# Optimization experiments

Hardware: AMD Instinct MI355X
Metric: run time of the kernel (lower is better)

## Reference

```python
import jax, jax.numpy as jnp
import numpy as np
import math

B, S, D, H = 2, 2048, 1024, 16

def setup_inputs() -> dict:
    key = jax.random.key(0)
    ks = jax.random.split(key, 13)
    def lin(kw, kb, out_d, in_d):
        W = jax.random.normal(kw, (out_d, in_d), dtype=jnp.float32) * 0.02
        b = jax.random.normal(kb, (out_d,), dtype=jnp.float32) * 0.02
        return W, b
    Wq, bq = lin(ks[0], ks[1], D, D)
    Wk, bk = lin(ks[2], ks[3], D, D)
    Wv, bv = lin(ks[4], ks[5], D, D)
    Wo, bo = lin(ks[6], ks[7], D, D)
    query = jax.random.normal(ks[8], (B, S, D), dtype=jnp.float32)
    key_t = jax.random.normal(ks[9], (B, S, D), dtype=jnp.float32)
    value = jax.random.normal(ks[10], (B, S, D), dtype=jnp.float32)
    src_mask = jax.random.randint(ks[11], (B, S), 0, 2).astype(bool)  # True = masked out
    return {"query": query, "key": key_t, "value": value, "src_mask": src_mask,
            "Wq": Wq, "bq": bq, "Wk": Wk, "bk": bk, "Wv": Wv, "bv": bv,
            "Wo": Wo, "bo": bo, "nhead": H}

def reference(query, key, value, src_mask, Wq, bq, Wk, bk, Wv, bv, Wo, bo, nhead):
    b, s, d = query.shape
    hd = d // nhead
    scale = 1.0 / math.sqrt(hd)
    def split_heads(x):  # [b,s,d] -> [b,h,s,hd]
        return x.reshape(b, -1, nhead, hd).transpose(0, 2, 1, 3)
    q = split_heads(query @ Wq.T + bq)
    k = split_heads(key @ Wk.T + bk)
    v = split_heads(value @ Wv.T + bv)
    scores = jnp.einsum('bhqe,bhke->bhqk', q, k) * scale  # [b,h,s,s]
    # mask True -> -9e9, broadcast over heads and query positions (matches repeat)
    scores = jnp.where(src_mask[:, None, None, :], jnp.float32(-9e9), scores)
    probs = jax.nn.softmax(scores, axis=-1)
    # dropout is identity in eval mode
    out = jnp.einsum('bhqk,bhke->bhqe', probs, v)  # [b,h,s,hd]
    out = out.transpose(0, 2, 1, 3).reshape(b, s, d)
    out = out @ Wo.T + bo
    return out
```

## Files before the change

### kernel.cpp

```cpp
#include <hip/hip_runtime.h>
#include <hip/hip_bf16.h>
#include <cstdint>
#include <cstddef>

#define B_ 2
#define S_ 2048
#define D_ 1024
#define H_ 16
#define HD_ 64
#define M_ 4096

typedef __attribute__((ext_vector_type(8))) short short8;
typedef __attribute__((ext_vector_type(4))) float floatx4;
typedef __attribute__((ext_vector_type(16))) float f32x16;
typedef __attribute__((ext_vector_type(2))) int intx2;

__device__ __forceinline__ floatx4 mfma32(short8 a, short8 b, floatx4 c) {
    return __builtin_amdgcn_mfma_f32_16x16x32_bf16(a, b, c, 0, 0, 0);
}
__device__ __forceinline__ f32x16 mfma3216(short8 a, short8 b, f32x16 c) {
    return __builtin_amdgcn_mfma_f32_32x32x16_bf16(a, b, c, 0, 0, 0);
}

__device__ __forceinline__ void gload_lds16(const __hip_bfloat16* g, __hip_bfloat16* lds_base) {
    __builtin_amdgcn_global_load_lds(
        (const __attribute__((address_space(1))) void*)g,
        (__attribute__((address_space(3))) void*)lds_base, 16, 0, 0);
}

__device__ __forceinline__ int pkbf(float a, float b) {
    union { __hip_bfloat162 h; int i; } u;
    u.h = __float22bfloat162_rn({a, b});
    return u.i;
}
__device__ __forceinline__ void pl32swap(int& a, int& b) {
    intx2 r = __builtin_amdgcn_permlane32_swap(a, b, false, false);
    a = r.x; b = r.y;
}

__global__ __launch_bounds__(256) void cvt_all_kernel(
    const float* __restrict__ q, const float* __restrict__ k, const float* __restrict__ v,
    const float* __restrict__ wq, const float* __restrict__ wk,
    const float* __restrict__ wv, const float* __restrict__ wo,
    const int* __restrict__ mask,
    __hip_bfloat16* __restrict__ dstIn,
    __hip_bfloat16* __restrict__ dstW,
    float* __restrict__ fbias)
{
    const int bid = blockIdx.x;
    const int tid = threadIdx.x;
    const size_t SZ_IN = (size_t)M_ * D_;
    const size_t SZ_W  = (size_t)D_ * D_;
    if (bid < 12288) {
        int z = bid >> 12, xb = bid & 4095;
        const float* src = z == 0 ? q : z == 1 ? k : v;
        __hip_bfloat16* d = dstIn + (size_t)z * SZ_IN;
        int i = (xb * 256 + tid) * 4;
        float4 val = *(const float4*)(src + i);
        union { __hip_bfloat16 h[4]; uint2 u; } cv;
        cv.h[0] = __float2bfloat16(val.x); cv.h[1] = __float2bfloat16(val.y);
        cv.h[2] = __float2bfloat16(val.z); cv.h[3] = __float2bfloat16(val.w);
        *(uint2*)(d + i) = cv.u;
    } else if (bid < 16384) {
        int r  = bid - 12288;
        int z  = r >> 10, xb = r & 1023;
        const float* src = z == 0 ? wq : z == 1 ? wk : z == 2 ? wv : wo;
        __hip_bfloat16* d = dstW + (size_t)z * SZ_W;
        int i = (xb * 256 + tid) * 4;
        float4 val = *(const float4*)(src + i);
        union { __hip_bfloat16 h[4]; uint2 u; } cv;
        cv.h[0] = __float2bfloat16(val.x); cv.h[1] = __float2bfloat16(val.y);
        cv.h[2] = __float2bfloat16(val.z); cv.h[3] = __float2bfloat16(val.w);
        *(uint2*)(d + i) = cv.u;
    } else {
        int i = ((bid - 16384) * 256 + tid) * 4;
        int4 m = *(const int4*)(mask + i);
        float4 o;
        o.x = m.x ? -100000.0f : 0.0f;
        o.y = m.y ? -100000.0f : 0.0f;
        o.z = m.z ? -100000.0f : 0.0f;
        o.w = m.w ? -100000.0f : 0.0f;
        *(float4*)(fbias + i) = o;
    }
}

template <int MODE>
__device__ __forceinline__ void gemm_core(
    const __hip_bfloat16* __restrict__ A,
    const __hip_bfloat16* __restrict__ W,
    const float* __restrict__ bias,
    void* __restrict__ Cout,
    __hip_bfloat16* __restrict__ smem,
    int m0, int n0, int N)
{
    __hip_bfloat16* As = smem;
    __hip_bfloat16* Bs = smem + 128 * 32;
    const int K = D_;
    const int tid  = threadIdx.x;
    const int wave = tid >> 6;
    const int lane = tid & 63;
    const int quad = lane >> 4;
    const int l15  = lane & 15;
    const int wm   = (wave & 1) * 64;
    const int wn   = (wave >> 1) * 64;
    const int srow = lane >> 2;
    const int scol = (lane & 3) * 8;

    floatx4 acc[4][4];
#pragma unroll
    for (int i = 0; i < 4; i++)
#pragma unroll
        for (int j = 0; j < 4; j++) {
            floatx4 z = {0.f, 0.f, 0.f, 0.f};
            acc[i][j] = z;
        }

    for (int k0 = 0; k0 < K; k0 += 32) {
        __syncthreads();
#pragma unroll
        for (int t = 0; t < 2; t++) {
            int r0 = wave * 32 + t * 16;
            gload_lds16(A + (size_t)(m0 + r0 + srow) * K + k0 + scol, As + r0 * 32);
            gload_lds16(W + (size_t)(n0 + r0 + srow) * K + k0 + scol, Bs + r0 * 32);
        }
        __syncthreads();

        short8 afr[4], bfr[4];
#pragma unroll
        for (int i = 0; i < 4; i++)
            afr[i] = *(const short8*)(As + (wm + i * 16 + l15) * 32 + quad * 8);
#pragma unroll
        for (int j = 0; j < 4; j++)
            bfr[j] = *(const short8*)(Bs + (wn + j * 16 + l15) * 32 + quad * 8);
#pragma unroll
        for (int i = 0; i < 4; i++)
#pragma unroll
            for (int j = 0; j < 4; j++)
                acc[i][j] = mfma32(afr[i], bfr[j], acc[i][j]);
    }

    if constexpr (MODE == 1) {
#pragma unroll
        for (int j = 0; j < 4; j++) {
            int col = n0 + wn + j * 16 + l15;
            int h = col >> 6, e = col & 63;
            float bv = bias[col];
#pragma unroll
            for (int i = 0; i < 4; i++) {
                int s0 = m0 + wm + i * 16 + quad * 4;
                int bb = s0 >> 11, sl = s0 & 2047;
                union { __hip_bfloat16 hx[4]; uint2 u; } pk;
#pragma unroll
                for (int r = 0; r < 4; r++)
                    pk.hx[r] = __float2bfloat16(acc[i][j][r] + bv);
                *(uint2*)((__hip_bfloat16*)Cout + (((size_t)bb * H_ + h) * HD_ + e) * S_ + sl) = pk.u;
            }
        }
    } else {
#pragma unroll
        for (int j = 0; j < 4; j++) {
            int col = n0 + wn + j * 16 + l15;
            float bv = bias[col];
#pragma unroll
            for (int i = 0; i < 4; i++) {
#pragma unroll
                for (int r = 0; r < 4; r++) {
                    int rowg = m0 + wm + i * 16 + quad * 4 + r;
                    ((__hip_bfloat16*)Cout)[(size_t)rowg * N + col] =
                        __float2bfloat16(acc[i][j][r] + bv);
                }
            }
        }
    }
}

__global__ __launch_bounds__(256) void qkv_gemm_kernel(
    const __hip_bfloat16* __restrict__ qb, const __hip_bfloat16* __restrict__ kb,
    const __hip_bfloat16* __restrict__ vb,
    const __hip_bfloat16* __restrict__ Wqb, const __hip_bfloat16* __restrict__ Wkb,
    const __hip_bfloat16* __restrict__ Wvb,
    const float* __restrict__ bq, const float* __restrict__ bk, const float* __restrict__ bv,
    __hip_bfloat16* __restrict__ Qp, __hip_bfloat16* __restrict__ Kp,
    __hip_bfloat16* __restrict__ Vt)
{
    __shared__ __hip_bfloat16 smem[2 * 128 * 32] __attribute__((aligned(16)));
    const int z = blockIdx.z;
    const __hip_bfloat16* A = z == 0 ? qb : z == 1 ? kb : vb;
    const __hip_bfloat16* W = z == 0 ? Wqb : z == 1 ? Wkb : Wvb;
    const float* bias = z == 0 ? bq : z == 1 ? bk : bv;
    int lin  = blockIdx.y * 8 + blockIdx.x;
    int work = (lin & 7) * 32 + (lin >> 3);
    int m0 = (work >> 3) * 128, n0 = (work & 7) * 128;
    if (z < 2) gemm_core<0>(A, W, bias, z == 0 ? (void*)Qp : (void*)Kp, smem, m0, n0, D_);
    else       gemm_core<1>(A, W, bias, (void*)Vt, smem, m0, n0, D_);
}

__global__ __launch_bounds__(256) void oproj_gemm_kernel(
    const __hip_bfloat16* __restrict__ A, const __hip_bfloat16* __restrict__ W,
    const float* __restrict__ bias, float* __restrict__ out)
{
    __shared__ __hip_bfloat16 As[64 * 32]  __attribute__((aligned(16)));
    __shared__ __hip_bfloat16 Bs[128 * 32] __attribute__((aligned(16)));
    const int K = D_, N = D_;
    const int tid  = threadIdx.x;
    int lin  = blockIdx.y * 8 + blockIdx.x;
    int work = (lin & 7) * 64 + (lin >> 3);
    const int m0   = (work >> 3) * 64;
    const int n0   = (work & 7) * 128;
    const int wave = tid >> 6;
    const int lane = tid & 63;
    const int quad = lane >> 4;
    const int l15  = lane & 15;
    const int wm   = (wave & 1) * 32;
    const int wn   = (wave >> 1) * 64;
    const int srow = lane >> 2;
    const int scol = (lane & 3) * 8;

    floatx4 acc[2][4];
#pragma unroll
    for (int i = 0; i < 2; i++)
#pragma unroll
        for (int j = 0; j < 4; j++) {
            floatx4 z = {0.f, 0.f, 0.f, 0.f};
            acc[i][j] = z;
        }

    for (int k0 = 0; k0 < K; k0 += 32) {
        __syncthreads();
        {
            int ra = wave * 16;
            gload_lds16(A + (size_t)(m0 + ra + srow) * K + k0 + scol, As + ra * 32);
#pragma unroll
            for (int t = 0; t < 2; t++) {
                int rb = wave * 32 + t * 16;
                gload_lds16(W + (size_t)(n0 + rb + srow) * K + k0 + scol, Bs + rb * 32);
            }
        }
        __syncthreads();

        short8 afr[2], bfr[4];
#pragma unroll
        for (int i = 0; i < 2; i++)
            afr[i] = *(const short8*)(As + (wm + i * 16 + l15) * 32 + quad * 8);
#pragma unroll
        for (int j = 0; j < 4; j++)
            bfr[j] = *(const short8*)(Bs + (wn + j * 16 + l15) * 32 + quad * 8);
#pragma unroll
        for (int i = 0; i < 2; i++)
#pragma unroll
            for (int j = 0; j < 4; j++)
                acc[i][j] = mfma32(afr[i], bfr[j], acc[i][j]);
    }

#pragma unroll
    for (int j = 0; j < 4; j++) {
        int col = n0 + wn + j * 16 + l15;
        float bv = bias[col];
#pragma unroll
        for (int i = 0; i < 2; i++) {
#pragma unroll
            for (int r = 0; r < 4; r++) {
                int rowg = m0 + wm + i * 16 + quad * 4 + r;
                out[(size_t)rowg * N + col] = acc[i][j][r] + bv;
            }
        }
    }
}

#define LDP 72
#define NTK (S_ / 64)
#define KVBUF (64 * LDP)
__global__ __launch_bounds__(512, 4) void flash_attn_kernel(
    const __hip_bfloat16* __restrict__ Q,
    const __hip_bfloat16* __restrict__ Kp,
    const __hip_bfloat16* __restrict__ Vt,
    const float* __restrict__ fbias,
    __hip_bfloat16* __restrict__ O)
{
    __shared__ __hip_bfloat16 smem[4 * KVBUF] __attribute__((aligned(16)));

    const int tid  = threadIdx.x;
    int lin  = blockIdx.y * 16 + blockIdx.x;
    int work = (lin & 7) * 64 + (lin >> 3);
    const int q0   = (work & 15) * 128;
    const int bh   = work >> 4;
    const int b    = bh >> 4;
    const int h    = bh & 15;
    const int warp = tid >> 6;
    const int qw   = warp & 3;
    const int kvh  = warp >> 2;
    const int lane = tid & 63;
    const int l31  = lane & 31;
    const int hi   = lane >> 5;
    const float kSc = 0.18033688f;

    const size_t baseQ = ((size_t)b * S_ + q0) * D_ + (size_t)h * HD_;
#pragma unroll
    for (int c = tid; c < 1024; c += 512) {
        int row = c >> 3, kc = c & 7;
        *(uint4*)(smem + row * LDP + kc * 8) =
            *(const uint4*)(Q + baseQ + (size_t)row * D_ + kc * 8);
    }
    __syncthreads();
    short8 qb[4];
#pragma unroll
    for (int ks = 0; ks < 4; ks++)
        qb[ks] = *(const short8*)(smem + (qw * 32 + l31) * LDP + ks * 16 + hi * 8);
    __syncthreads();

    const float* brow = fbias + b * S_;
    const __hip_bfloat16* VtBase = Vt + (size_t)bh * HD_ * S_;
    const size_t baseKrow = (size_t)b * S_ * D_ + (size_t)h * HD_;

    const int r0  = tid >> 3;
    const int kc0 = (tid & 7) * 8;

    uint4 kreg, vreg;
    auto issue = [&](int kv0) {
        kreg = *(const uint4*)(Kp + baseKrow + (size_t)(kv0 + r0) * D_ + kc0);
        vreg = *(const uint4*)(VtBase + (size_t)r0 * S_ + kv0 + kc0);
    };
    auto commit = [&](int pb) {
        *(uint4*)(smem + pb * KVBUF + r0 * LDP + kc0) = kreg;
        *(uint4*)(smem + (2 + pb) * KVBUF + r0 * LDP + kc0) = vreg;
    };

    issue(0);
    commit(0);
    __syncthreads();

    float lsum = 0.f;
    f32x16 o_acc[2];
#pragma unroll
    for (int hdb = 0; hdb < 2; hdb++)
#pragma unroll
        for (int r = 0; r < 16; r++) o_acc[hdb][r] = 0.f;

    short8 pa_p[2];
    short8 vfr_p[4];

    for (int t = 0; t < NTK; ++t) {
        if (t) __syncthreads();

        if (t + 1 < NTK) issue((t + 1) * 64);

        const __hip_bfloat16* Ks  = smem + (t & 1) * KVBUF;
        const __hip_bfloat16* Vts = smem + (2 + (t & 1)) * KVBUF;

        f32x16 z;
#pragma unroll
        for (int r = 0; r < 16; r++) z[r] = 0.f;
        __builtin_amdgcn_s_setprio(1);
#pragma unroll
        for (int ks = 0; ks < 4; ks++) {
            short8 ka = *(const short8*)(Ks + (kvh * 32 + l31) * LDP + ks * 16 + hi * 8);
            z = mfma3216(ka, qb[ks], z);
        }
        if (t) {
#pragma unroll
            for (int hdb = 0; hdb < 2; hdb++)
#pragma unroll
                for (int ksl = 0; ksl < 2; ksl++)
                    o_acc[hdb] = mfma3216(pa_p[ksl], vfr_p[hdb * 2 + ksl], o_acc[hdb]);
        }
        __builtin_amdgcn_s_setprio(0);

#pragma unroll
        for (int ksl = 0; ksl < 2; ksl++) {
            const float* bb = brow + t * 64 + kvh * 32 + ksl * 16 + hi * 4;
            floatx4 b0 = *(const floatx4*)(bb);
            floatx4 b1 = *(const floatx4*)(bb + 8);
            float p[8];
#pragma unroll
            for (int i = 0; i < 8; i++) {
                float bias = (i < 4) ? b0[i & 3] : b1[i & 3];
                p[i] = __builtin_amdgcn_exp2f(z[ksl * 8 + i] * kSc + bias);
            }
            lsum += ((p[0] + p[1]) + (p[2] + p[3])) + ((p[4] + p[5]) + (p[6] + p[7]));
            int w0 = pkbf(p[0], p[1]);
            int w2 = pkbf(p[4], p[5]);
            int w1 = pkbf(p[2], p[3]);
            int w3 = pkbf(p[6], p[7]);
            pl32swap(w0, w2);
            pl32swap(w1, w3);
            union { int w[4]; short8 s; } fr;
            fr.w[0] = w0; fr.w[1] = w1; fr.w[2] = w2; fr.w[3] = w3;
            pa_p[ksl] = fr.s;
        }

#pragma unroll
        for (int hdb = 0; hdb < 2; hdb++)
#pragma unroll
            for (int ksl = 0; ksl < 2; ksl++)
                vfr_p[hdb * 2 + ksl] = *(const short8*)(Vts + (hdb * 32 + l31) * LDP +
                                                        kvh * 32 + ksl * 16 + hi * 8);

        if (t + 1 < NTK) commit((t + 1) & 1);
    }

    __builtin_amdgcn_s_setprio(1);
#pragma unroll
    for (int hdb = 0; hdb < 2; hdb++)
#pragma unroll
        for (int ksl = 0; ksl < 2; ksl++)
            o_acc[hdb] = mfma3216(pa_p[ksl], vfr_p[hdb * 2 + ksl], o_acc[hdb]);
    __builtin_amdgcn_s_setprio(0);

    __syncthreads();
    float* ored = (float*)smem;
    float* lred = (float*)smem + 8192;
    if (kvh == 1) {
#pragma unroll
        for (int hdb = 0; hdb < 2; hdb++)
#pragma unroll
            for (int r = 0; r < 16; r++)
                ored[(hdb * 16 + r) * 256 + qw * 64 + lane] = o_acc[hdb][r];
        lred[qw * 64 + lane] = lsum;
    }
    __syncthreads();
    if (kvh == 0) {
#pragma unroll
        for (int hdb = 0; hdb < 2; hdb++)
#pragma unroll
            for (int r = 0; r < 16; r++)
                o_acc[hdb][r] += ored[(hdb * 16 + r) * 256 + qw * 64 + lane];
        float ls = lsum + lred[qw * 64 + lane];
        ls += __shfl_xor(ls, 32);
        float inv = 1.0f / ls;

        const size_t baseO = ((size_t)b * S_ + q0 + qw * 32) * D_ + (size_t)h * HD_;
#pragma unroll
        for (int r = 0; r < 16; r++) {
            int crow = (r & 3) + 8 * (r >> 2) + 4 * hi;
            float iv = __shfl(inv, crow);
#pragma unroll
            for (int hdb = 0; hdb < 2; hdb++)
                O[baseO + (size_t)crow * D_ + hdb * 32 + l31] =
                    __float2bfloat16(o_acc[hdb][r] * iv);
        }
    }
}

extern "C" void kernel_launch(void* const* d_in, const int* in_sizes, int n_in,
                              void* d_out, int out_size, void* d_ws, size_t ws_size,
                              hipStream_t stream) {
    const float* query = (const float*)d_in[0];
    const float* key   = (const float*)d_in[1];
    const float* value = (const float*)d_in[2];
    const int*   mask  = (const int*)d_in[3];
    const float* Wq    = (const float*)d_in[4];
    const float* bq    = (const float*)d_in[5];
    const float* Wk    = (const float*)d_in[6];
    const float* bk    = (const float*)d_in[7];
    const float* Wv    = (const float*)d_in[8];
    const float* bv    = (const float*)d_in[9];
    const float* Wo    = (const float*)d_in[10];
    const float* bo    = (const float*)d_in[11];
    float* out = (float*)d_out;

    const size_t SZ_IN = (size_t)M_ * D_;
    const size_t SZ_W  = (size_t)D_ * D_;
    __hip_bfloat16* qb  = (__hip_bfloat16*)d_ws;
    __hip_bfloat16* kb  = qb  + SZ_IN;
    __hip_bfloat16* vb  = kb  + SZ_IN;
    __hip_bfloat16* Wqb = vb  + SZ_IN;
    __hip_bfloat16* Wkb = Wqb + SZ_W;
    __hip_bfloat16* Wvb = Wkb + SZ_W;
    __hip_bfloat16* Wob = Wvb + SZ_W;
    __hip_bfloat16* Qp  = Wob + SZ_W;
    __hip_bfloat16* Kp  = Qp  + SZ_IN;
    __hip_bfloat16* Vt  = Kp  + SZ_IN;
    float*          fb  = (float*)(Vt + SZ_IN);

    cvt_all_kernel<<<dim3(16388), 256, 0, stream>>>(
        query, key, value, Wq, Wk, Wv, Wo, mask, qb, Wqb, fb);

    qkv_gemm_kernel<<<dim3(D_ / 128, M_ / 128, 3), 256, 0, stream>>>(
        qb, kb, vb, Wqb, Wkb, Wvb, bq, bk, bv, Qp, Kp, Vt);

    flash_attn_kernel<<<dim3(S_ / 128, B_ * H_), 512, 0, stream>>>(Qp, Kp, Vt, fb, Qp);

    oproj_gemm_kernel<<<dim3(D_ / 128, M_ / 64), 256, 0, stream>>>(Qp, Wob, bo, out);
}
```

Before: 221.7 us.

## Double the flash-attention KV tile to 128 and drop cross-iteration PV software pipelining

The flash attention loop now processes 128 keys per iteration instead of 64, halving the number of barriers and global-to-LDS staging rounds. Each iteration runs two QK^T MFMA chains and interleaves softmax packing with the PV MFMAs, reading V fragments straight from LDS rather than carrying P and V fragments over to the next iteration. This raises register and LDS use (two prefetch registers each for K and V, larger buffers) and gives up the previous overlap of last iteration's PV with the current QK^T.

New measurement: 271.3 us. +22.4%, slower.

```diff
diff --git a/kernel.cpp b/kernel.cpp
--- a/kernel.cpp
+++ b/kernel.cpp
@@ -267,9 +267,37 @@
     }
 }
 
-#define LDP 72
-#define NTK (S_ / 64)
-#define KVBUF (64 * LDP)
+__device__ __forceinline__ void sm_pack(const f32x16& z, const float* brow_sub, int hi,
+                                        float kSc, float& lsum, short8* pa) {
+#pragma unroll
+    for (int ksl = 0; ksl < 2; ksl++) {
+        const float* bb = brow_sub + ksl * 16 + hi * 4;
+        floatx4 b0 = *(const floatx4*)(bb);
+        floatx4 b1 = *(const floatx4*)(bb + 8);
+        float p[8];
+#pragma unroll
+        for (int i = 0; i < 8; i++) {
+            float bias = (i < 4) ? b0[i & 3] : b1[i & 3];
+            p[i] = __builtin_amdgcn_exp2f(z[ksl * 8 + i] * kSc + bias);
+        }
+        lsum += ((p[0] + p[1]) + (p[2] + p[3])) + ((p[4] + p[5]) + (p[6] + p[7]));
+        int w0 = pkbf(p[0], p[1]);
+        int w2 = pkbf(p[4], p[5]);
+        int w1 = pkbf(p[2], p[3]);
+        int w3 = pkbf(p[6], p[7]);
+        pl32swap(w0, w2);
+        pl32swap(w1, w3);
+        union { int w[4]; short8 s; } fr;
+        fr.w[0] = w0; fr.w[1] = w1; fr.w[2] = w2; fr.w[3] = w3;
+        pa[ksl] = fr.s;
+    }
+}
+
+#define LDPK 72
+#define LDPV 136
+#define KTILE 128
+#define NT2 (S_ / KTILE)
+#define BUFSZ (KTILE * LDPK + HD_ * LDPV)
 __global__ __launch_bounds__(512, 4) void flash_attn_kernel(
     const __hip_bfloat16* __restrict__ Q,
     const __hip_bfloat16* __restrict__ Kp,
@@ -277,7 +305,7 @@
     const float* __restrict__ fbias,
     __hip_bfloat16* __restrict__ O)
 {
-    __shared__ __hip_bfloat16 smem[4 * KVBUF] __attribute__((aligned(16)));
+    __shared__ __hip_bfloat16 smem[2 * BUFSZ] __attribute__((aligned(16)));
 
     const int tid  = threadIdx.x;
     int lin  = blockIdx.y * 16 + blockIdx.x;
@@ -298,31 +326,39 @@
 #pragma unroll
     for (int c = tid; c < 1024; c += 512) {
         int row = c >> 3, kc = c & 7;
-        *(uint4*)(smem + row * LDP + kc * 8) =
+        *(uint4*)(smem + row * LDPK + kc * 8) =
             *(const uint4*)(Q + baseQ + (size_t)row * D_ + kc * 8);
     }
     __syncthreads();
     short8 qb[4];
 #pragma unroll
     for (int ks = 0; ks < 4; ks++)
-        qb[ks] = *(const short8*)(smem + (qw * 32 + l31) * LDP + ks * 16 + hi * 8);
+        qb[ks] = *(const short8*)(smem + (qw * 32 + l31) * LDPK + ks * 16 + hi * 8);
     __syncthreads();
 
     const float* brow = fbias + b * S_;
     const __hip_bfloat16* VtBase = Vt + (size_t)bh * HD_ * S_;
     const size_t baseKrow = (size_t)b * S_ * D_ + (size_t)h * HD_;
 
-    const int r0  = tid >> 3;
-    const int kc0 = (tid & 7) * 8;
-
-    uint4 kreg, vreg;
+    const int kr  = tid >> 3;
+    const int kcc = (tid & 7) * 8;
+    const int vr  = tid >> 4;
+    const int vcc = (tid & 15) * 8;
+
+    uint4 kreg[2], vreg[2];
     auto issue = [&](int kv0) {
-        kreg = *(const uint4*)(Kp + baseKrow + (size_t)(kv0 + r0) * D_ + kc0);
-        vreg = *(const uint4*)(VtBase + (size_t)r0 * S_ + kv0 + kc0);
+        kreg[0] = *(const uint4*)(Kp + baseKrow + (size_t)(kv0 + kr) * D_ + kcc);
+        kreg[1] = *(const uint4*)(Kp + baseKrow + (size_t)(kv0 + kr + 64) * D_ + kcc);
+        vreg[0] = *(const uint4*)(VtBase + (size_t)vr * S_ + kv0 + vcc);
+        vreg[1] = *(const uint4*)(VtBase + (size_t)(vr + 32) * S_ + kv0 + vcc);
     };
     auto commit = [&](int pb) {
-        *(uint4*)(smem + pb * KVBUF + r0 * LDP + kc0) = kreg;
-        *(uint4*)(smem + (2 + pb) * KVBUF + r0 * LDP + kc0) = vreg;
+        __hip_bfloat16* kb2 = smem + pb * BUFSZ;
+        __hip_bfloat16* vb2 = smem + pb * BUFSZ + KTILE * LDPK;
+        *(uint4*)(kb2 + kr * LDPK + kcc) = kreg[0];
+        *(uint4*)(kb2 + (kr + 64) * LDPK + kcc) = kreg[1];
+        *(uint4*)(vb2 + vr * LDPV + vcc) = vreg[0];
+        *(uint4*)(vb2 + (vr + 32) * LDPV + vcc) = vreg[1];
     };
 
     issue(0);
@@ -336,75 +372,56 @@
 #pragma unroll
         for (int r = 0; r < 16; r++) o_acc[hdb][r] = 0.f;
 
-    short8 pa_p[2];
-    short8 vfr_p[4];
-
-    for (int t = 0; t < NTK; ++t) {
+    for (int t = 0; t < NT2; ++t) {
         if (t) __syncthreads();
 
-        if (t + 1 < NTK) issue((t + 1) * 64);
-
-        const __hip_bfloat16* Ks  = smem + (t & 1) * KVBUF;
-        const __hip_bfloat16* Vts = smem + (2 + (t & 1)) * KVBUF;
-
-        f32x16 z;
-#pragma unroll
-        for (int r = 0; r < 16; r++) z[r] = 0.f;
+        if (t + 1 < NT2) issue((t + 1) * KTILE);
+
+        const __hip_bfloat16* Ks  = smem + (t & 1) * BUFSZ;
+        const __hip_bfloat16* Vts = smem + (t & 1) * BUFSZ + KTILE * LDPK;
+
+        f32x16 za, zb;
+#pragma unroll
+        for (int r = 0; r < 16; r++) { za[r] = 0.f; zb[r] = 0.f; }
         __builtin_amdgcn_s_setprio(1);
 #pragma unroll
         for (int ks = 0; ks < 4; ks++) {
-            short8 ka = *(const short8*)(Ks + (kvh * 32 + l31) * LDP + ks * 16 + hi * 8);
-            z = mfma3216(ka, qb[ks], z);
-        }
-        if (t) {
-#pragma unroll
-            for (int hdb = 0; hdb < 2; hdb++)
-#pragma unroll
-                for (int ksl = 0; ksl < 2; ksl++)
-                    o_acc[hdb] = mfma3216(pa_p[ksl], vfr_p[hdb * 2 + ksl], o_acc[hdb]);
+            short8 ka = *(const short8*)(Ks + (kvh * 32 + l31) * LDPK + ks * 16 + hi * 8);
+            za = mfma3216(ka, qb[ks], za);
+        }
+#pragma unroll
+        for (int ks = 0; ks < 4; ks++) {
+            short8 ka = *(const short8*)(Ks + (64 + kvh * 32 + l31) * LDPK + ks * 16 + hi * 8);
+            zb = mfma3216(ka, qb[ks], zb);
         }
         __builtin_amdgcn_s_setprio(0);
 
-#pragma unroll
-        for (int ksl = 0; ksl < 2; ksl++) {
-            const float* bb = brow + t * 64 + kvh * 32 + ksl * 16 + hi * 4;
-            floatx4 b0 = *(const floatx4*)(bb);
-            floatx4 b1 = *(const floatx4*)(bb + 8);
-            float p[8];
-#pragma unroll
-            for (int i = 0; i < 8; i++) {
-                float bias = (i < 4) ? b0[i & 3] : b1[i & 3];
-                p[i] = __builtin_amdgcn_exp2f(z[ksl * 8 + i] * kSc + bias);
+        short8 pa[2];
+        sm_pack(za, brow + t * KTILE + kvh * 32, hi, kSc, lsum, pa);
+        __builtin_amdgcn_s_setprio(1);
+#pragma unroll
+        for (int hdb = 0; hdb < 2; hdb++)
+#pragma unroll
+            for (int ksl = 0; ksl < 2; ksl++) {
+                short8 vf = *(const short8*)(Vts + (hdb * 32 + l31) * LDPV +
+                                             kvh * 32 + ksl * 16 + hi * 8);
+                o_acc[hdb] = mfma3216(pa[ksl], vf, o_acc[hdb]);
             }
-            lsum += ((p[0] + p[1]) + (p[2] + p[3])) + ((p[4] + p[5]) + (p[6] + p[7]));
-            int w0 = pkbf(p[0], p[1]);
-            int w2 = pkbf(p[4], p[5]);
-            int w1 = pkbf(p[2], p[3]);
-            int w3 = pkbf(p[6], p[7]);
-            pl32swap(w0, w2);
-            pl32swap(w1, w3);
-            union { int w[4]; short8 s; } fr;
-            fr.w[0] = w0; fr.w[1] = w1; fr.w[2] = w2; fr.w[3] = w3;
-            pa_p[ksl] = fr.s;
-        }
-
+        __builtin_amdgcn_s_setprio(0);
+        sm_pack(zb, brow + t * KTILE + 64 + kvh * 32, hi, kSc, lsum, pa);
+        __builtin_amdgcn_s_setprio(1);
 #pragma unroll
         for (int hdb = 0; hdb < 2; hdb++)
 #pragma unroll
-            for (int ksl = 0; ksl < 2; ksl++)
-                vfr_p[hdb * 2 + ksl] = *(const short8*)(Vts + (hdb * 32 + l31) * LDP +
-                                                        kvh * 32 + ksl * 16 + hi * 8);
-
-        if (t + 1 < NTK) commit((t + 1) & 1);
-    }
-
-    __builtin_amdgcn_s_setprio(1);
-#pragma unroll
-    for (int hdb = 0; hdb < 2; hdb++)
-#pragma unroll
-        for (int ksl = 0; ksl < 2; ksl++)
-            o_acc[hdb] = mfma3216(pa_p[ksl], vfr_p[hdb * 2 + ksl], o_acc[hdb]);
-    __builtin_amdgcn_s_setprio(0);
+            for (int ksl = 0; ksl < 2; ksl++) {
+                short8 vf = *(const short8*)(Vts + (hdb * 32 + l31) * LDPV +
+                                             64 + kvh * 32 + ksl * 16 + hi * 8);
+                o_acc[hdb] = mfma3216(pa[ksl], vf, o_acc[hdb]);
+            }
+        __builtin_amdgcn_s_setprio(0);
+
+        if (t + 1 < NT2) commit((t + 1) & 1);
+    }
 
     __syncthreads();
     float* ored = (float*)smem;
```
